# Optimization experiments

Measured on AMD Instinct MI355X. Metric: run time of the kernel, lower is better.

The kernel has to match this reference:

```python
import jax, jax.numpy as jnp
import numpy as np

LN2 = jnp.log(jnp.float32(2.0))
ALPHA = 0.5          # alpha_pool = [0.5]
A_BITS = 8           # activation bit width (BIT_TYPE_A)
W_BITS = 8           # weight bit width (BIT_TYPE_W)
EPS = 1e-8


def round_ln(x):
    # 'round' branch: floor(log2(x)) then pick nearer power of two
    y = jnp.floor(jnp.log(x) / LN2)
    up = (x - 2.0 ** y) > (2.0 ** (y + 1.0) - x)
    return y + up.astype(x.dtype)


def fq_act_asym(x, bits=A_BITS):
    # per-tensor asymmetric uniform fake-quant (QAct min-max observer)
    qmax = 2 ** bits - 1
    xmin = jnp.minimum(x.min(), 0.0)
    xmax = jnp.maximum(x.max(), 0.0)
    scale = jnp.maximum((xmax - xmin) / qmax, EPS)
    zp = jnp.round(-xmin / scale)
    q = jnp.clip(jnp.round(x / scale) + zp, 0, qmax)
    return (q - zp) * scale


def fq_act_sym(x, bits=A_BITS):
    # per-tensor symmetric fake-quant (qact1 with asymmetric=False)
    qmax = 2 ** (bits - 1) - 1
    scale = jnp.maximum(jnp.abs(x).max() / qmax, EPS)
    q = jnp.clip(jnp.round(x / scale), -qmax - 1, qmax)
    return q * scale


def fq_weight(w, bits=W_BITS):
    # per-output-channel symmetric weight fake-quant (QLinear)
    qmax = 2 ** (bits - 1) - 1
    scale = jnp.maximum(jnp.abs(w).max(axis=1, keepdims=True) / qmax, EPS)
    q = jnp.clip(jnp.round(w / scale), -qmax - 1, qmax)
    return q * scale


def setup_inputs() -> dict:
    key = jax.random.key(0)
    ks = jax.random.split(key, 5)
    B, N, C, H = 64, 197, 768, 3072
    x = jax.random.normal(ks[0], (B, N, C), dtype=jnp.float32)
    w1 = jax.random.normal(ks[1], (H, C), dtype=jnp.float32) * 0.02
    b1 = jax.random.normal(ks[2], (H,), dtype=jnp.float32) * 0.02
    w2 = jax.random.normal(ks[3], (C, H), dtype=jnp.float32) * 0.02
    b2 = jax.random.normal(ks[4], (C,), dtype=jnp.float32) * 0.02
    return {"x": x, "w1": w1, "b1": b1, "w2": w2, "b2": b2}


def reference(x, w1, b1, w2, b2):
    # ---- smoothquant power-of-two channel scale (fc1 input channels) ----
    global_max_x = jnp.abs(x).max(axis=(0, 1))      # [C]
    max_weight = jnp.abs(w1).max(axis=0)            # [C]
    cs = global_max_x ** ALPHA / max_weight ** (1.0 - ALPHA)
    cs = 2.0 ** round_ln(cs)                        # snap to power of two
    x_smoothed = x / cs[None, None, :]
    w1_smoothed = w1 * cs[None, :]
    # ---- qact0 -> fc1 (8-bit fake-quant GEMM) ----
    xq = fq_act_asym(x_smoothed)
    h = jnp.einsum('bnc,hc->bnh', xq, fq_weight(w1_smoothed)) + b1
    # ---- act (exact GELU, nn.GELU default) -> qact1 (symmetric) ----
    h = jax.nn.gelu(h, approximate=False)
    hq = fq_act_sym(h)
    # ---- fc2 -> qact2 ----
    out = jnp.einsum('bnh,ch->bnc', hq, fq_weight(w2)) + b2
    out = fq_act_asym(out)
    return out
```

## Files before the change

kernel.cpp:

```cpp
#include <hip/hip_runtime.h>
#include <cstdint>
#include <cstddef>

typedef int v4i __attribute__((ext_vector_type(4)));

#define DI static __device__ __forceinline__

DI unsigned fmap(float f){ unsigned b=__float_as_uint(f); return (b&0x80000000u)? ~b : (b|0x80000000u); }
DI float funmap(unsigned u){ return (u&0x80000000u)? __uint_as_float(u&0x7fffffffu) : __uint_as_float(~u); }
DI float gelu_f(float x){ return 0.5f*x*(1.0f+erff(x*0.70710678118654752440f)); }

constexpr int Mtok = 12608;
constexpr int Cdim = 768;
constexpr int Hdim = 3072;
constexpr int MP   = 12672;

__global__ void k_init(unsigned* scal, unsigned* xminU, unsigned* xmaxU, unsigned* wmaxU){
    int t = blockIdx.x*256 + threadIdx.x;
    if (t < Cdim){
        xminU[t] = fmap(__builtin_inff());
        xmaxU[t] = fmap(-__builtin_inff());
        wmaxU[t] = fmap(0.0f);
    }
    if (t == 0){
        scal[0] = fmap(0.0f);
        scal[1] = fmap(__builtin_inff());
        scal[2] = fmap(-__builtin_inff());
    }
}

__global__ void k_colstats_x(const float* __restrict__ x, unsigned* xminU, unsigned* xmaxU){
    int t = threadIdx.x;
    float mn0= __builtin_inff(), mn1= __builtin_inff(), mn2= __builtin_inff();
    float mx0=-__builtin_inff(), mx1=-__builtin_inff(), mx2=-__builtin_inff();
    for (int r = blockIdx.x; r < Mtok; r += gridDim.x){
        const float* row = x + (size_t)r*Cdim;
        float v0=row[t], v1=row[t+256], v2=row[t+512];
        mn0=fminf(mn0,v0); mx0=fmaxf(mx0,v0);
        mn1=fminf(mn1,v1); mx1=fmaxf(mx1,v1);
        mn2=fminf(mn2,v2); mx2=fmaxf(mx2,v2);
    }
    atomicMin(&xminU[t      ], fmap(mn0)); atomicMax(&xmaxU[t      ], fmap(mx0));
    atomicMin(&xminU[t+256  ], fmap(mn1)); atomicMax(&xmaxU[t+256  ], fmap(mx1));
    atomicMin(&xminU[t+512  ], fmap(mn2)); atomicMax(&xmaxU[t+512  ], fmap(mx2));
}

__global__ void k_colmax_w1(const float* __restrict__ w1, unsigned* wmaxU){
    int t = threadIdx.x;
    float m0=0.f, m1=0.f, m2=0.f;
    for (int r = blockIdx.x; r < Hdim; r += gridDim.x){
        const float* row = w1 + (size_t)r*Cdim;
        m0=fmaxf(m0,fabsf(row[t]));
        m1=fmaxf(m1,fabsf(row[t+256]));
        m2=fmaxf(m2,fabsf(row[t+512]));
    }
    atomicMax(&wmaxU[t      ], fmap(m0));
    atomicMax(&wmaxU[t+256  ], fmap(m1));
    atomicMax(&wmaxU[t+512  ], fmap(m2));
}

__global__ void k_scale0(const unsigned* xminU, const unsigned* xmaxU, const unsigned* wmaxU,
                         float* cs, unsigned* scal){
    __shared__ float smn[256], smx[256];
    int t = threadIdx.x;
    float lmn =  __builtin_inff(), lmx = -__builtin_inff();
    #pragma unroll
    for (int j = 0; j < 3; ++j){
        int c = t + j*256;
        float xn = funmap(xminU[c]), xm = funmap(xmaxU[c]), wm = funmap(wmaxU[c]);
        float g  = fmaxf(fabsf(xn), fabsf(xm));
        float csr = powf(g, 0.5f) / powf(wm, 0.5f);
        float y = floorf(logf(csr) / 0.6931471805599453f);
        float p = exp2f(y);
        float c2 = exp2f(y + (((csr - p) > (2.0f*p - csr)) ? 1.0f : 0.0f));
        cs[c] = c2;
        lmn = fminf(lmn, xn / c2);
        lmx = fmaxf(lmx, xm / c2);
    }
    smn[t]=lmn; smx[t]=lmx; __syncthreads();
    for (int s=128; s; s>>=1){
        if (t < s){ smn[t]=fminf(smn[t],smn[t+s]); smx[t]=fmaxf(smx[t],smx[t+s]); }
        __syncthreads();
    }
    if (t == 0){
        float xmin_t = fminf(smn[0], 0.0f);
        float xmax_t = fmaxf(smx[0], 0.0f);
        float sc = fmaxf((xmax_t - xmin_t)/255.0f, 1e-8f);
        float zp = rintf(-xmin_t/sc);
        float* fs = (float*)scal;
        fs[8] = sc; fs[9] = zp;
    }
}

__global__ void k_quant_w1(const float* __restrict__ w1, const float* __restrict__ cs,
                           const unsigned* scal, int8_t* __restrict__ qw1,
                           float* sa1, int* icorr1){
    __shared__ float sm[256];
    __shared__ int   si[256];
    int h = blockIdx.x, t = threadIdx.x;
    const float* wr = w1 + (size_t)h*Cdim;
    float v0 = wr[t]*cs[t], v1 = wr[t+256]*cs[t+256], v2 = wr[t+512]*cs[t+512];
    float am = fmaxf(fabsf(v0), fmaxf(fabsf(v1), fabsf(v2)));
    sm[t]=am; __syncthreads();
    for (int s=128; s; s>>=1){ if (t<s) sm[t]=fmaxf(sm[t],sm[t+s]); __syncthreads(); }
    float scale = fmaxf(sm[0]/127.0f, 1e-8f);
    float q0 = fminf(fmaxf(rintf(v0/scale), -128.0f), 127.0f);
    float q1 = fminf(fmaxf(rintf(v1/scale), -128.0f), 127.0f);
    float q2 = fminf(fmaxf(rintf(v2/scale), -128.0f), 127.0f);
    qw1[(size_t)h*Cdim + t      ] = (int8_t)q0;
    qw1[(size_t)h*Cdim + t + 256] = (int8_t)q1;
    qw1[(size_t)h*Cdim + t + 512] = (int8_t)q2;
    si[t] = (int)q0 + (int)q1 + (int)q2; __syncthreads();
    for (int s=128; s; s>>=1){ if (t<s) si[t]+=si[t+s]; __syncthreads(); }
    if (t == 0){
        const float* fs = (const float*)scal;
        sa1[h]    = fs[8]*scale;
        icorr1[h] = (128 - (int)fs[9]) * si[0];
    }
}

__global__ void k_quant_w2(const float* __restrict__ w2, int8_t* __restrict__ qw2, float* sa2){
    __shared__ float sm[256];
    int c = blockIdx.x, t = threadIdx.x;
    const float* wr = w2 + (size_t)c*Hdim;
    float v[12]; float am = 0.f;
    #pragma unroll
    for (int j=0;j<12;++j){ v[j]=wr[t + j*256]; am=fmaxf(am,fabsf(v[j])); }
    sm[t]=am; __syncthreads();
    for (int s=128; s; s>>=1){ if (t<s) sm[t]=fmaxf(sm[t],sm[t+s]); __syncthreads(); }
    float scale = fmaxf(sm[0]/127.0f, 1e-8f);
    #pragma unroll
    for (int j=0;j<12;++j){
        float q = fminf(fmaxf(rintf(v[j]/scale), -128.0f), 127.0f);
        qw2[(size_t)c*Hdim + t + j*256] = (int8_t)q;
    }
    if (t == 0) sa2[c] = scale;
}

__global__ void k_quant_x(const float* __restrict__ x, const float* __restrict__ cs,
                          const unsigned* scal, int8_t* __restrict__ qxs){
    int idx = blockIdx.x*256 + threadIdx.x;
    const int total = Mtok*(Cdim/4);
    if (idx >= total) return;
    const float* fs = (const float*)scal;
    float sc = fs[8], zp = fs[9];
    float4 v = ((const float4*)x)[idx];
    int cb = (idx % (Cdim/4))*4;
    float q0 = fminf(fmaxf(rintf((v.x/cs[cb+0])/sc)+zp, 0.f), 255.f);
    float q1 = fminf(fmaxf(rintf((v.y/cs[cb+1])/sc)+zp, 0.f), 255.f);
    float q2 = fminf(fmaxf(rintf((v.z/cs[cb+2])/sc)+zp, 0.f), 255.f);
    float q3 = fminf(fmaxf(rintf((v.w/cs[cb+3])/sc)+zp, 0.f), 255.f);
    uint32_t pack =  (uint32_t)(uint8_t)((int)q0-128)
                  | ((uint32_t)(uint8_t)((int)q1-128) << 8)
                  | ((uint32_t)(uint8_t)((int)q2-128) << 16)
                  | ((uint32_t)(uint8_t)((int)q3-128) << 24);
    ((uint32_t*)qxs)[idx] = pack;
}

#define GLL(src,dst) __builtin_amdgcn_global_load_lds( \
    (const __attribute__((address_space(1))) unsigned*)(src), \
    (__attribute__((address_space(3))) unsigned*)(dst), 16, 0, 0)

template<int KSTEPS, int MODE, int NY>
__global__ __launch_bounds__(256)
void k_gemm(const int8_t* __restrict__ A, const int8_t* __restrict__ Bw, int N,
            const float* __restrict__ sa, const int* __restrict__ icorr,
            const float* __restrict__ bias, const unsigned* __restrict__ scal,
            int8_t* __restrict__ qout, float* __restrict__ fout, _Float16* __restrict__ hout,
            unsigned* __restrict__ r0, unsigned* __restrict__ r1)
{
    constexpr int K = KSTEPS*64;
    __shared__ __align__(16) int8_t As0[8192];
    __shared__ __align__(16) int8_t Bs0[8192];
    __shared__ __align__(16) int8_t As1[8192];
    __shared__ __align__(16) int8_t Bs1[8192];
    __shared__ float sred[8];
    int t = threadIdx.x, lane = t & 63, wid = t >> 6;
    int wr = wid >> 1, wc = wid & 1;

    int nwg = gridDim.x;
    int q8 = nwg >> 3, r8 = nwg & 7;
    int xcd = blockIdx.x & 7, li = blockIdx.x >> 3;
    int swz = (xcd < r8 ? xcd*(q8+1) : r8*(q8+1) + (xcd - r8)*q8) + li;
    int bx = swz / NY, by = swz % NY;
    size_t brow = (size_t)bx * 128;
    int bcol = by * 128;

    int srow = t >> 2;
    int schunk = (t & 3) ^ ((srow >> 1) & 3);
    const int8_t* ga0 = A  + (brow + srow)*(size_t)K + schunk*16;
    const int8_t* gb0 = Bw + (size_t)(bcol + srow)*K + schunk*16;

    int rsw  = ((lane >> 4) ^ ((lane >> 1) & 3)) << 4;
    int aoff = ((wr*64 + (lane & 15)) << 6) + rsw;
    int boff = ((wc*64 + (lane & 15)) << 6) + rsw;

    v4i acc[4][4] = {};

#define STAGE(AS,BS,ks) do{ \
    const int8_t* pa_ = ga0 + (ks)*64; \
    const int8_t* pb_ = gb0 + (ks)*64; \
    GLL(pa_,                   AS + t*16); \
    GLL(pa_ + (size_t)64*K,    AS + 4096 + t*16); \
    GLL(pb_,                   BS + t*16); \
    GLL(pb_ + (size_t)64*K,    BS + 4096 + t*16); \
}while(0)

#define COMPUTE(AS,BS) do{ \
    v4i a_[4], b_[4]; \
    _Pragma("unroll") \
    for (int m=0;m<4;++m) a_[m] = *(const v4i*)(AS + aoff + (m<<10)); \
    _Pragma("unroll") \
    for (int n=0;n<4;++n) b_[n] = *(const v4i*)(BS + boff + (n<<10)); \
    _Pragma("unroll") \
    for (int m=0;m<4;++m) \
        _Pragma("unroll") \
        for (int n=0;n<4;++n) \
            acc[m][n] = __builtin_amdgcn_mfma_i32_16x16x64_i8(a_[m], b_[n], acc[m][n], 0, 0, 0); \
}while(0)

    STAGE(As0,Bs0,0);
    __syncthreads();
    for (int ks = 0; ks < KSTEPS; ks += 2){
        STAGE(As1,Bs1,ks+1);
        COMPUTE(As0,Bs0);
        __syncthreads();
        if (ks + 2 < KSTEPS) STAGE(As0,Bs0,ks+2);
        COMPUTE(As1,Bs1);
        __syncthreads();
    }

    int rl = (lane >> 4) * 4;
    if (MODE == 0){
        float amax = 0.f;
        #pragma unroll
        for (int n=0;n<4;++n){
            int col = bcol + wc*64 + n*16 + (lane & 15);
            float s = sa[col]; int ic = icorr[col]; float bb = bias[col];
            #pragma unroll
            for (int m=0;m<4;++m){
                size_t row = brow + wr*64 + m*16 + rl;
                #pragma unroll
                for (int r=0;r<4;++r){
                    if (row + r < (size_t)Mtok){
                        float g = gelu_f(s*(float)(acc[m][n][r] + ic) + bb);
                        amax = fmaxf(amax, fabsf(g));
                    }
                }
            }
        }
        #pragma unroll
        for (int off=32; off; off>>=1) amax = fmaxf(amax, __shfl_down(amax, off));
        if (lane == 0) sred[wid] = amax;
        __syncthreads();
        if (t == 0) atomicMax(r0, fmap(fmaxf(fmaxf(sred[0],sred[1]), fmaxf(sred[2],sred[3]))));
    } else if (MODE == 1){
        float sh = fmaxf(funmap(*scal)/127.0f, 1e-8f);
        #pragma unroll
        for (int n=0;n<4;++n){
            int col = bcol + wc*64 + n*16 + (lane & 15);
            float s = sa[col]; int ic = icorr[col]; float bb = bias[col];
            #pragma unroll
            for (int m=0;m<4;++m){
                size_t row = brow + wr*64 + m*16 + rl;
                #pragma unroll
                for (int r=0;r<4;++r){
                    if (row + r < (size_t)Mtok){
                        float g = gelu_f(s*(float)(acc[m][n][r] + ic) + bb);
                        float qv = fminf(fmaxf(rintf(g/sh), -128.0f), 127.0f);
                        qout[(row + r)*(size_t)N + col] = (int8_t)qv;
                    }
                }
            }
        }
    } else if (MODE == 3){
        float amax = 0.f;
        #pragma unroll
        for (int n=0;n<4;++n){
            int col = bcol + wc*64 + n*16 + (lane & 15);
            float s = sa[col]; int ic = icorr[col]; float bb = bias[col];
            #pragma unroll
            for (int m=0;m<4;++m){
                size_t row = brow + wr*64 + m*16 + rl;
                #pragma unroll
                for (int r=0;r<4;++r){
                    if (row + r < (size_t)Mtok){
                        float g = gelu_f(s*(float)(acc[m][n][r] + ic) + bb);
                        amax = fmaxf(amax, fabsf(g));
                        hout[(row + r)*(size_t)N + col] = (_Float16)g;
                    }
                }
            }
        }
        #pragma unroll
        for (int off=32; off; off>>=1) amax = fmaxf(amax, __shfl_down(amax, off));
        if (lane == 0) sred[wid] = amax;
        __syncthreads();
        if (t == 0) atomicMax(r0, fmap(fmaxf(fmaxf(sred[0],sred[1]), fmaxf(sred[2],sred[3]))));
    } else {
        float sh = fmaxf(funmap(*scal)/127.0f, 1e-8f);
        float lmin =  __builtin_inff(), lmax = -__builtin_inff();
        #pragma unroll
        for (int n=0;n<4;++n){
            int col = bcol + wc*64 + n*16 + (lane & 15);
            float s = sh * sa[col]; float bb = bias[col];
            #pragma unroll
            for (int m=0;m<4;++m){
                size_t row = brow + wr*64 + m*16 + rl;
                #pragma unroll
                for (int r=0;r<4;++r){
                    if (row + r < (size_t)Mtok){
                        float o = s*(float)acc[m][n][r] + bb;
                        fout[(row + r)*(size_t)N + col] = o;
                        lmin = fminf(lmin, o); lmax = fmaxf(lmax, o);
                    }
                }
            }
        }
        #pragma unroll
        for (int off=32; off; off>>=1){
            lmin = fminf(lmin, __shfl_down(lmin, off));
            lmax = fmaxf(lmax, __shfl_down(lmax, off));
        }
        if (lane == 0){ sred[wid] = lmin; sred[4+wid] = lmax; }
        __syncthreads();
        if (t == 0){
            atomicMin(r0, fmap(fminf(fminf(sred[0],sred[1]), fminf(sred[2],sred[3]))));
            atomicMax(r1, fmap(fmaxf(fmaxf(sred[4],sred[5]), fmaxf(sred[6],sred[7]))));
        }
    }
#undef STAGE
#undef COMPUTE
}

struct alignas(16) H8 { _Float16 v[8]; };
__global__ void k_requant(const _Float16* __restrict__ h, const unsigned* __restrict__ scal,
                          int8_t* __restrict__ qh){
    int idx = blockIdx.x*256 + threadIdx.x;
    const int total = Mtok*(Hdim/8);
    if (idx >= total) return;
    float sh = fmaxf(funmap(scal[0])/127.0f, 1e-8f);
    H8 h8 = ((const H8*)h)[idx];
    uint32_t lo = 0, hi = 0;
    #pragma unroll
    for (int j=0;j<4;++j){
        float qv = fminf(fmaxf(rintf((float)h8.v[j]/sh), -128.0f), 127.0f);
        lo |= ((uint32_t)(uint8_t)(int)qv) << (8*j);
    }
    #pragma unroll
    for (int j=0;j<4;++j){
        float qv = fminf(fmaxf(rintf((float)h8.v[4+j]/sh), -128.0f), 127.0f);
        hi |= ((uint32_t)(uint8_t)(int)qv) << (8*j);
    }
    uint2 pk; pk.x = lo; pk.y = hi;
    ((uint2*)qh)[idx] = pk;
}

__global__ void k_final(const float* __restrict__ outpre, const unsigned* __restrict__ scal,
                        float* __restrict__ out){
    int idx = blockIdx.x*256 + threadIdx.x;
    const int total = Mtok*(Cdim/4);
    if (idx >= total) return;
    float omin = fminf(funmap(scal[1]), 0.0f);
    float omax = fmaxf(funmap(scal[2]), 0.0f);
    float sc = fmaxf((omax - omin)/255.0f, 1e-8f);
    float zp = rintf(-omin/sc);
    float4 v = ((const float4*)outpre)[idx];
    v.x = (fminf(fmaxf(rintf(v.x/sc)+zp, 0.f), 255.f) - zp)*sc;
    v.y = (fminf(fmaxf(rintf(v.y/sc)+zp, 0.f), 255.f) - zp)*sc;
    v.z = (fminf(fmaxf(rintf(v.z/sc)+zp, 0.f), 255.f) - zp)*sc;
    v.w = (fminf(fmaxf(rintf(v.w/sc)+zp, 0.f), 255.f) - zp)*sc;
    ((float4*)out)[idx] = v;
}

extern "C" void kernel_launch(void* const* d_in, const int* in_sizes, int n_in,
                              void* d_out, int out_size, void* d_ws, size_t ws_size,
                              hipStream_t stream)
{
    if (n_in < 5) return;
    const float* x  = (const float*)d_in[0];
    const float* w1 = (const float*)d_in[1];
    const float* b1 = (const float*)d_in[2];
    const float* w2 = (const float*)d_in[3];
    const float* b2 = (const float*)d_in[4];
    float* out = (float*)d_out;

    uint8_t* w = (uint8_t*)d_ws;
    size_t off = 0;
    unsigned* scal  = (unsigned*)(w + off); off += 256;
    unsigned* xminU = (unsigned*)(w + off); off += 3072;
    unsigned* xmaxU = (unsigned*)(w + off); off += 3072;
    unsigned* wmaxU = (unsigned*)(w + off); off += 3072;
    float*    cs    = (float*)   (w + off); off += 3072;
    float*    sa1   = (float*)   (w + off); off += 12288;
    int*      icorr1= (int*)     (w + off); off += 12288;
    float*    sa2   = (float*)   (w + off); off += 3072;
    off = (off + 255) & ~(size_t)255;
    int8_t*   qw1   = (int8_t*)  (w + off); off += (size_t)Hdim*Cdim;
    int8_t*   qw2   = (int8_t*)  (w + off); off += (size_t)Cdim*Hdim;
    int8_t*   qxs   = (int8_t*)  (w + off); off += (size_t)MP*Cdim;
    int8_t*   qh    = (int8_t*)  (w + off); off += (size_t)MP*Hdim;
    size_t off_big = off;
    float*    outpre= (float*)   (w + off_big);
    _Float16* hbuf  = (_Float16*)(w + off_big);
    size_t need_3g  = off_big + (size_t)Mtok*Cdim*4;
    size_t need_h16 = off_big + (size_t)Mtok*Hdim*2;
    if (ws_size < need_3g) return;
    bool use_h16 = (ws_size >= need_h16);

    k_init<<<3, 256, 0, stream>>>(scal, xminU, xmaxU, wmaxU);
    k_colstats_x<<<512, 256, 0, stream>>>(x, xminU, xmaxU);
    k_colmax_w1<<<512, 256, 0, stream>>>(w1, wmaxU);
    k_scale0<<<1, 256, 0, stream>>>(xminU, xmaxU, wmaxU, cs, scal);
    k_quant_w1<<<Hdim, 256, 0, stream>>>(w1, cs, scal, qw1, sa1, icorr1);
    k_quant_w2<<<Cdim, 256, 0, stream>>>(w2, qw2, sa2);
    k_quant_x<<<(Mtok*(Cdim/4) + 255)/256, 256, 0, stream>>>(x, cs, scal, qxs);

    if (use_h16){
        k_gemm<12,3,24><<<2376, 256, 0, stream>>>(qxs, qw1, Hdim, sa1, icorr1, b1, scal,
                                                  nullptr, nullptr, hbuf, &scal[0], nullptr);
        k_requant<<<(Mtok*(Hdim/8) + 255)/256, 256, 0, stream>>>(hbuf, scal, qh);
    } else {
        k_gemm<12,0,24><<<2376, 256, 0, stream>>>(qxs, qw1, Hdim, sa1, icorr1, b1, scal,
                                                  nullptr, nullptr, nullptr, &scal[0], nullptr);
        k_gemm<12,1,24><<<2376, 256, 0, stream>>>(qxs, qw1, Hdim, sa1, icorr1, b1, scal,
                                                  qh, nullptr, nullptr, nullptr, nullptr);
    }
    k_gemm<48,2,6><<<594, 256, 0, stream>>>(qh, qw2, Cdim, sa2, nullptr, b2, scal,
                                            nullptr, outpre, nullptr, &scal[1], &scal[2]);

    k_final<<<(Mtok*(Cdim/4) + 255)/256, 256, 0, stream>>>(outpre, scal, out);
}
```

Before: 382.0 us.

## Triple-buffer GEMM LDS pipeline and store epilogue in tile-blocked layout

```diff
diff --git a/kernel.cpp b/kernel.cpp
--- a/kernel.cpp
+++ b/kernel.cpp
@@ -161,6 +161,10 @@
     (const __attribute__((address_space(1))) unsigned*)(src), \
     (__attribute__((address_space(3))) unsigned*)(dst), 16, 0, 0)
 
+#define WAITVM8 asm volatile("s_waitcnt vmcnt(8)" ::: "memory")
+#define WAITVM4 asm volatile("s_waitcnt vmcnt(4)" ::: "memory")
+#define WAITVM0 asm volatile("s_waitcnt vmcnt(0)" ::: "memory")
+
 template<int KSTEPS, int MODE, int NY>
 __global__ __launch_bounds__(256)
 void k_gemm(const int8_t* __restrict__ A, const int8_t* __restrict__ Bw, int N,
@@ -170,10 +174,7 @@
             unsigned* __restrict__ r0, unsigned* __restrict__ r1)
 {
     constexpr int K = KSTEPS*64;
-    __shared__ __align__(16) int8_t As0[8192];
-    __shared__ __align__(16) int8_t Bs0[8192];
-    __shared__ __align__(16) int8_t As1[8192];
-    __shared__ __align__(16) int8_t Bs1[8192];
+    __shared__ __align__(16) int8_t LDSB[49152];
     __shared__ float sred[8];
     int t = threadIdx.x, lane = t & 63, wid = t >> 6;
     int wr = wid >> 1, wc = wid & 1;
@@ -193,57 +194,79 @@
 
     int rsw  = ((lane >> 4) ^ ((lane >> 1) & 3)) << 4;
     int aoff = ((wr*64 + (lane & 15)) << 6) + rsw;
-    int boff = ((wc*64 + (lane & 15)) << 6) + rsw;
-
-    v4i acc[4][4] = {};
-
-#define STAGE(AS,BS,ks) do{ \
+    int boff = 8192 + ((wc*64 + (lane & 15)) << 6) + rsw;
+
+    float sav[4], bbv[4]; int icv[4]; float sh = 0.f;
+    #pragma unroll
+    for (int n=0;n<4;++n){
+        int col = bcol + wc*64 + n*16 + (lane & 15);
+        sav[n] = sa[col];
+        bbv[n] = bias[col];
+        icv[n] = (MODE == 2) ? 0 : icorr[col];
+    }
+    if (MODE == 1 || MODE == 2) sh = fmaxf(funmap(*scal)/127.0f, 1e-8f);
+    asm volatile("" ::: "memory");
+
+#define STAGE(cur, ks) do{ \
     const int8_t* pa_ = ga0 + (ks)*64; \
     const int8_t* pb_ = gb0 + (ks)*64; \
-    GLL(pa_,                   AS + t*16); \
-    GLL(pa_ + (size_t)64*K,    AS + 4096 + t*16); \
-    GLL(pb_,                   BS + t*16); \
-    GLL(pb_ + (size_t)64*K,    BS + 4096 + t*16); \
+    int8_t* ld_ = LDSB + (cur)*16384 + t*16; \
+    GLL(pa_,                ld_); \
+    GLL(pa_ + (size_t)64*K, ld_ + 4096); \
+    GLL(pb_,                ld_ + 8192); \
+    GLL(pb_ + (size_t)64*K, ld_ + 12288); \
 }while(0)
 
-#define COMPUTE(AS,BS) do{ \
+    v4i acc[4][4] = {};
+    STAGE(0,0); STAGE(1,1); STAGE(2,2);
+
+#define ITER(cur, ks, WAITM, RESTAGE) do{ \
+    WAITM;                                    \
+    __builtin_amdgcn_s_barrier();             \
+    const int8_t* bp_ = LDSB + (cur)*16384; \
     v4i a_[4], b_[4]; \
     _Pragma("unroll") \
-    for (int m=0;m<4;++m) a_[m] = *(const v4i*)(AS + aoff + (m<<10)); \
+    for (int m_=0;m_<4;++m_) a_[m_] = *(const v4i*)(bp_ + aoff + (m_<<10)); \
     _Pragma("unroll") \
-    for (int n=0;n<4;++n) b_[n] = *(const v4i*)(BS + boff + (n<<10)); \
+    for (int n_=0;n_<4;++n_) b_[n_] = *(const v4i*)(bp_ + boff + (n_<<10)); \
+    asm volatile("s_waitcnt lgkmcnt(0)" ::: "memory"); \
+    __builtin_amdgcn_sched_barrier(0); \
+    __builtin_amdgcn_s_barrier();             \
+    if (RESTAGE) STAGE(cur, (ks)+3); \
+    __builtin_amdgcn_s_setprio(1); \
     _Pragma("unroll") \
-    for (int m=0;m<4;++m) \
+    for (int m_=0;m_<4;++m_) \
         _Pragma("unroll") \
-        for (int n=0;n<4;++n) \
-            acc[m][n] = __builtin_amdgcn_mfma_i32_16x16x64_i8(a_[m], b_[n], acc[m][n], 0, 0, 0); \
+        for (int n_=0;n_<4;++n_) \
+            acc[m_][n_] = __builtin_amdgcn_mfma_i32_16x16x64_i8(a_[m_], b_[n_], acc[m_][n_], 0, 0, 0); \
+    __builtin_amdgcn_s_setprio(0); \
 }while(0)
 
-    STAGE(As0,Bs0,0);
-    __syncthreads();
-    for (int ks = 0; ks < KSTEPS; ks += 2){
-        STAGE(As1,Bs1,ks+1);
-        COMPUTE(As0,Bs0);
-        __syncthreads();
-        if (ks + 2 < KSTEPS) STAGE(As0,Bs0,ks+2);
-        COMPUTE(As1,Bs1);
-        __syncthreads();
-    }
+    constexpr int MAING = (KSTEPS - 3)/3;
+    for (int kg = 0; kg < MAING; ++kg){
+        int ks = kg*3;
+        ITER(0, ks,   WAITVM8, true);
+        ITER(1, ks+1, WAITVM8, true);
+        ITER(2, ks+2, WAITVM8, true);
+    }
+    ITER(0, KSTEPS-3, WAITVM8, false);
+    ITER(1, KSTEPS-2, WAITVM4, false);
+    ITER(2, KSTEPS-1, WAITVM0, false);
+#undef ITER
+#undef STAGE
 
     int rl = (lane >> 4) * 4;
     if (MODE == 0){
         float amax = 0.f;
         #pragma unroll
         for (int n=0;n<4;++n){
-            int col = bcol + wc*64 + n*16 + (lane & 15);
-            float s = sa[col]; int ic = icorr[col]; float bb = bias[col];
             #pragma unroll
             for (int m=0;m<4;++m){
                 size_t row = brow + wr*64 + m*16 + rl;
                 #pragma unroll
                 for (int r=0;r<4;++r){
                     if (row + r < (size_t)Mtok){
-                        float g = gelu_f(s*(float)(acc[m][n][r] + ic) + bb);
+                        float g = gelu_f(sav[n]*(float)(acc[m][n][r] + icv[n]) + bbv[n]);
                         amax = fmaxf(amax, fabsf(g));
                     }
                 }
@@ -255,18 +278,16 @@
         __syncthreads();
         if (t == 0) atomicMax(r0, fmap(fmaxf(fmaxf(sred[0],sred[1]), fmaxf(sred[2],sred[3]))));
     } else if (MODE == 1){
-        float sh = fmaxf(funmap(*scal)/127.0f, 1e-8f);
         #pragma unroll
         for (int n=0;n<4;++n){
             int col = bcol + wc*64 + n*16 + (lane & 15);
-            float s = sa[col]; int ic = icorr[col]; float bb = bias[col];
             #pragma unroll
             for (int m=0;m<4;++m){
                 size_t row = brow + wr*64 + m*16 + rl;
                 #pragma unroll
                 for (int r=0;r<4;++r){
                     if (row + r < (size_t)Mtok){
-                        float g = gelu_f(s*(float)(acc[m][n][r] + ic) + bb);
+                        float g = gelu_f(sav[n]*(float)(acc[m][n][r] + icv[n]) + bbv[n]);
                         float qv = fminf(fmaxf(rintf(g/sh), -128.0f), 127.0f);
                         qout[(row + r)*(size_t)N + col] = (int8_t)qv;
                     }
@@ -275,21 +296,20 @@
         }
     } else if (MODE == 3){
         float amax = 0.f;
+        _Float16* hb = hout + ((size_t)(bx*NY + by))*16384 + (size_t)t*64;
         #pragma unroll
         for (int n=0;n<4;++n){
-            int col = bcol + wc*64 + n*16 + (lane & 15);
-            float s = sa[col]; int ic = icorr[col]; float bb = bias[col];
             #pragma unroll
             for (int m=0;m<4;++m){
                 size_t row = brow + wr*64 + m*16 + rl;
+                union { _Float16 h4[4]; uint2 u2; } pk;
                 #pragma unroll
                 for (int r=0;r<4;++r){
-                    if (row + r < (size_t)Mtok){
-                        float g = gelu_f(s*(float)(acc[m][n][r] + ic) + bb);
-                        amax = fmaxf(amax, fabsf(g));
-                        hout[(row + r)*(size_t)N + col] = (_Float16)g;
-                    }
+                    float g = gelu_f(sav[n]*(float)(acc[m][n][r] + icv[n]) + bbv[n]);
+                    if (row + r < (size_t)Mtok) amax = fmaxf(amax, fabsf(g));
+                    pk.h4[r] = (_Float16)g;
                 }
+                ((uint2*)hb)[n*4 + m] = pk.u2;
             }
         }
         #pragma unroll
@@ -298,23 +318,22 @@
         __syncthreads();
         if (t == 0) atomicMax(r0, fmap(fmaxf(fmaxf(sred[0],sred[1]), fmaxf(sred[2],sred[3]))));
     } else {
-        float sh = fmaxf(funmap(*scal)/127.0f, 1e-8f);
         float lmin =  __builtin_inff(), lmax = -__builtin_inff();
+        float* ob = fout + ((size_t)(bx*NY + by))*16384 + (size_t)t*64;
         #pragma unroll
         for (int n=0;n<4;++n){
-            int col = bcol + wc*64 + n*16 + (lane & 15);
-            float s = sh * sa[col]; float bb = bias[col];
+            float s = sh * sav[n];
             #pragma unroll
             for (int m=0;m<4;++m){
                 size_t row = brow + wr*64 + m*16 + rl;
+                float4 o4;
                 #pragma unroll
                 for (int r=0;r<4;++r){
-                    if (row + r < (size_t)Mtok){
-                        float o = s*(float)acc[m][n][r] + bb;
-                        fout[(row + r)*(size_t)N + col] = o;
-                        lmin = fminf(lmin, o); lmax = fmaxf(lmax, o);
-                    }
+                    float o = s*(float)acc[m][n][r] + bbv[n];
+                    if (row + r < (size_t)Mtok){ lmin = fminf(lmin, o); lmax = fmaxf(lmax, o); }
+                    ((float*)&o4)[r] = o;
                 }
+                ((float4*)ob)[n*4 + m] = o4;
             }
         }
         #pragma unroll
@@ -329,28 +348,32 @@
             atomicMax(r1, fmap(fmaxf(fmaxf(sred[4],sred[5]), fmaxf(sred[6],sred[7]))));
         }
     }
-#undef STAGE
-#undef COMPUTE
-}
-
-struct alignas(16) H8 { _Float16 v[8]; };
+}
+
 __global__ void k_requant(const _Float16* __restrict__ h, const unsigned* __restrict__ scal,
                           int8_t* __restrict__ qh){
     int idx = blockIdx.x*256 + threadIdx.x;
     const int total = Mtok*(Hdim/8);
     if (idx >= total) return;
     float sh = fmaxf(funmap(scal[0])/127.0f, 1e-8f);
-    H8 h8 = ((const H8*)h)[idx];
+    int R  = idx / 384;
+    int cb = (idx - R*384) * 8;
+    int bx = R >> 7, r0 = R & 127;
+    int by = cb >> 7;
+    int wr = r0 >> 6, m = (r0 >> 4) & 3, lhi = (r0 >> 2) & 3, r = r0 & 3;
+    int wc = (cb >> 6) & 1, n = (cb >> 4) & 3, li0 = cb & 15;
+    int tb = (wr*2 + wc)*64 + lhi*16 + li0;
+    const _Float16* p = h + ((size_t)(bx*24 + by))*16384 + (size_t)tb*64 + ((n*4 + m)*4 + r);
     uint32_t lo = 0, hi = 0;
     #pragma unroll
     for (int j=0;j<4;++j){
-        float qv = fminf(fmaxf(rintf((float)h8.v[j]/sh), -128.0f), 127.0f);
-        lo |= ((uint32_t)(uint8_t)(int)qv) << (8*j);
+        float q = fminf(fmaxf(rintf((float)p[j*64]/sh), -128.0f), 127.0f);
+        lo |= ((uint32_t)(uint8_t)(int)q) << (8*j);
     }
     #pragma unroll
     for (int j=0;j<4;++j){
-        float qv = fminf(fmaxf(rintf((float)h8.v[4+j]/sh), -128.0f), 127.0f);
-        hi |= ((uint32_t)(uint8_t)(int)qv) << (8*j);
+        float q = fminf(fmaxf(rintf((float)p[(4+j)*64]/sh), -128.0f), 127.0f);
+        hi |= ((uint32_t)(uint8_t)(int)q) << (8*j);
     }
     uint2 pk; pk.x = lo; pk.y = hi;
     ((uint2*)qh)[idx] = pk;
@@ -365,7 +388,16 @@
     float omax = fmaxf(funmap(scal[2]), 0.0f);
     float sc = fmaxf((omax - omin)/255.0f, 1e-8f);
     float zp = rintf(-omin/sc);
-    float4 v = ((const float4*)outpre)[idx];
+    int R  = idx / 192;
+    int cb = (idx - R*192) * 4;
+    int bx = R >> 7, r0 = R & 127;
+    int by = cb >> 7;
+    int wr = r0 >> 6, m = (r0 >> 4) & 3, lhi = (r0 >> 2) & 3, r = r0 & 3;
+    int wc = (cb >> 6) & 1, n = (cb >> 4) & 3, li0 = cb & 15;
+    int tb = (wr*2 + wc)*64 + lhi*16 + li0;
+    const float* p = outpre + ((size_t)(bx*6 + by))*16384 + (size_t)tb*64 + ((n*4 + m)*4 + r);
+    float4 v;
+    v.x = p[0]; v.y = p[64]; v.z = p[128]; v.w = p[192];
     v.x = (fminf(fmaxf(rintf(v.x/sc)+zp, 0.f), 255.f) - zp)*sc;
     v.y = (fminf(fmaxf(rintf(v.y/sc)+zp, 0.f), 255.f) - zp)*sc;
     v.z = (fminf(fmaxf(rintf(v.z/sc)+zp, 0.f), 255.f) - zp)*sc;
@@ -403,8 +435,8 @@
     size_t off_big = off;
     float*    outpre= (float*)   (w + off_big);
     _Float16* hbuf  = (_Float16*)(w + off_big);
-    size_t need_3g  = off_big + (size_t)Mtok*Cdim*4;
-    size_t need_h16 = off_big + (size_t)Mtok*Hdim*2;
+    size_t need_3g  = off_big + (size_t)99*6*16384*4;
+    size_t need_h16 = off_big + (size_t)99*24*16384*2;
     if (ws_size < need_3g) return;
     bool use_h16 = (ws_size >= need_h16);
 
```

Measured after the change: 387.5 us. About the same (+1.4%).
